# Kernel tuning notes

Hardware: AMD Instinct MI355X
Metric: run time of the kernel (lower is better)

The kernel has to match this reference:

```python
import jax, jax.numpy as jnp
import numpy as np

N, E = 50000, 800000
IN_DIM, HIDDEN, HEADS, EDGE_DIM, OUT_DIM = 128, 64, 4, 16, 1
NEG_SLOPE = 0.2


def gat_conv(x, src, dst, edge_attr, W, We, att_src, att_dst, att_edge, bias, heads, out_ch, concat):
    n = x.shape[0]
    h = (x @ W).reshape(n, heads, out_ch)                     # [N,H,C]
    a_src = jnp.einsum('nhc,hc->nh', h, att_src)              # [N,H]
    a_dst = jnp.einsum('nhc,hc->nh', h, att_dst)
    e = (edge_attr @ We).reshape(-1, heads, out_ch)           # [E,H,C]
    a_e = jnp.einsum('ehc,hc->eh', e, att_edge)               # [E,H]
    alpha = jax.nn.leaky_relu(a_src[src] + a_dst[dst] + a_e, NEG_SLOPE)  # [E,H]
    # per-destination-node softmax
    amax = jax.ops.segment_max(alpha, dst, num_segments=n)
    ex = jnp.exp(alpha - amax[dst])
    denom = jax.ops.segment_sum(ex, dst, num_segments=n)
    alpha = ex / (denom[dst] + 1e-16)
    msg = h[src] * alpha[..., None]                           # [E,H,C]
    out = jax.ops.segment_sum(msg, dst, num_segments=n)       # [N,H,C]
    out = out.reshape(n, heads * out_ch) if concat else out.mean(axis=1)
    return out + bias


def setup_inputs() -> dict:
    key = jax.random.key(0)
    ks = jax.random.split(key, 16)
    s = 0.1
    inp = {
        'x': jax.random.normal(ks[0], (N, IN_DIM), jnp.float32),
        'edge_index': jax.random.randint(ks[1], (2, E), 0, N, jnp.int32),
        'edge_attr': jax.random.normal(ks[2], (E, EDGE_DIM), jnp.float32),
        # layer 1: heads=4, concat=True
        'W1': jax.random.normal(ks[3], (IN_DIM, HEADS * HIDDEN), jnp.float32) * s,
        'We1': jax.random.normal(ks[4], (EDGE_DIM, HEADS * HIDDEN), jnp.float32) * s,
        'as1': jax.random.normal(ks[5], (HEADS, HIDDEN), jnp.float32) * s,
        'ad1': jax.random.normal(ks[6], (HEADS, HIDDEN), jnp.float32) * s,
        'ae1': jax.random.normal(ks[7], (HEADS, HIDDEN), jnp.float32) * s,
        'b1': jnp.zeros((HEADS * HIDDEN,), jnp.float32),
        # layer 2: heads=1, concat=False
        'W2': jax.random.normal(ks[8], (HEADS * HIDDEN, HIDDEN), jnp.float32) * s,
        'We2': jax.random.normal(ks[9], (EDGE_DIM, HIDDEN), jnp.float32) * s,
        'as2': jax.random.normal(ks[10], (1, HIDDEN), jnp.float32) * s,
        'ad2': jax.random.normal(ks[11], (1, HIDDEN), jnp.float32) * s,
        'ae2': jax.random.normal(ks[12], (1, HIDDEN), jnp.float32) * s,
        'b2': jnp.zeros((HIDDEN,), jnp.float32),
        'Wlin': jax.random.normal(ks[13], (HIDDEN, OUT_DIM), jnp.float32) * s,
        'blin': jnp.zeros((OUT_DIM,), jnp.float32),
    }
    return inp


def reference(x, edge_index, edge_attr, W1, We1, as1, ad1, ae1, b1, W2, We2, as2, ad2, ae2, b2, Wlin, blin):
    src, dst = edge_index[0], edge_index[1]
    h = jax.nn.relu(gat_conv(x, src, dst, edge_attr, W1, We1, as1, ad1, ae1, b1, HEADS, HIDDEN, True))
    h = jax.nn.relu(gat_conv(h, src, dst, edge_attr, W2, We2, as2, ad2, ae2, b2, 1, HIDDEN, False))
    return h @ Wlin + blin
```

## Files before the change

kernel.cpp:

```cpp
#include <hip/hip_runtime.h>
#include <math.h>

#define IN_DIM 128
#define HID 64
#define HEADS 4
#define EDGE_DIM 16
#define L1_OUT 256
#define NEG_SLOPE 0.2f
#define PAD 64

typedef __attribute__((ext_vector_type(8))) _Float16 half8_t;
typedef __attribute__((ext_vector_type(4))) _Float16 half4_t;
typedef __attribute__((ext_vector_type(4))) float floatx4;

struct __align__(16) Rec16 {
    int src;
    float aeq2;
    _Float16 e1[4];
};

__global__ __launch_bounds__(256) void prep_kernel(
    const float* __restrict__ W1, const float* __restrict__ as1, const float* __restrict__ ad1,
    const float* __restrict__ W2, const float* __restrict__ as2, const float* __restrict__ ad2,
    const float* __restrict__ We1, const float* __restrict__ ae1,
    const float* __restrict__ We2, const float* __restrict__ ae2,
    _Float16* __restrict__ W1t, _Float16* __restrict__ W2t,
    float* __restrict__ q1, float* __restrict__ q2,
    int* __restrict__ deg, int Nn) {
    int id = blockIdx.x * 256 + threadIdx.x;
    if (id < Nn) deg[id] = 0;
    if (id < 272 * 128) {
        int n = id >> 7, k = id & 127;
        float v = 0.f;
        if (n < 256) v = W1[k * 256 + n];
        else if (n < 260) { int h = n - 256; float s = 0.f;
            for (int c = 0; c < 64; ++c) s += W1[k * 256 + h * 64 + c] * as1[h * 64 + c]; v = s; }
        else if (n < 264) { int h = n - 260; float s = 0.f;
            for (int c = 0; c < 64; ++c) s += W1[k * 256 + h * 64 + c] * ad1[h * 64 + c]; v = s; }
        W1t[id] = (_Float16)v;
        return;
    }
    id -= 272 * 128;
    if (id < 80 * 256) {
        int n = id >> 8, k = id & 255;
        float v = 0.f;
        if (n < 64) v = W2[k * 64 + n];
        else if (n == 64) { float s = 0.f; for (int c = 0; c < 64; ++c) s += W2[k * 64 + c] * as2[c]; v = s; }
        else if (n == 65) { float s = 0.f; for (int c = 0; c < 64; ++c) s += W2[k * 64 + c] * ad2[c]; v = s; }
        W2t[id] = (_Float16)v;
        return;
    }
    id -= 80 * 256;
    if (id < 64) {
        int k = id >> 2, h = id & 3;
        float s = 0.f;
        for (int c = 0; c < 64; ++c) s += We1[k * 256 + h * 64 + c] * ae1[h * 64 + c];
        q1[id] = s;
        return;
    }
    id -= 64;
    if (id < 16) {
        float s = 0.f;
        for (int c = 0; c < 64; ++c) s += We2[id * 64 + c] * ae2[c];
        q2[id] = s;
    }
}

__global__ __launch_bounds__(256) void scatter_edge_kernel(
    const int* __restrict__ src, const int* __restrict__ dst,
    const float* __restrict__ ea, const float* __restrict__ q1,
    const float* __restrict__ q2, const float* __restrict__ asrc1,
    const float* __restrict__ adst1, int* __restrict__ deg,
    floatx4* __restrict__ rec, int E) {
    __shared__ float q[80];
    if (threadIdx.x < 64) q[threadIdx.x] = q1[threadIdx.x];
    else if (threadIdx.x < 80) q[threadIdx.x] = q2[threadIdx.x - 64];
    __syncthreads();
    int e = blockIdx.x * 256 + threadIdx.x;
    if (e >= E) return;
    const floatx4* p = (const floatx4*)(ea + (size_t)e * EDGE_DIM);
    floatx4 v0 = __builtin_nontemporal_load(p);
    floatx4 v1 = __builtin_nontemporal_load(p + 1);
    floatx4 v2 = __builtin_nontemporal_load(p + 2);
    floatx4 v3 = __builtin_nontemporal_load(p + 3);
    int sn = src[e];
    int d = dst[e];
    float4 as4 = *(const float4*)(asrc1 + (size_t)sn * 4);
    float4 ad4 = *(const float4*)(adst1 + (size_t)d * 4);
    float a[16] = {v0.x, v0.y, v0.z, v0.w, v1.x, v1.y, v1.z, v1.w,
                   v2.x, v2.y, v2.z, v2.w, v3.x, v3.y, v3.z, v3.w};
    Rec16 rc;
    rc.src = sn;
    float r2s = 0.f;
#pragma unroll
    for (int k = 0; k < 16; ++k) r2s += a[k] * q[64 + k];
    rc.aeq2 = r2s;
    const float* asp = (const float*)&as4;
    const float* adp = (const float*)&ad4;
#pragma unroll
    for (int h = 0; h < 4; ++h) {
        float s = 0.f;
#pragma unroll
        for (int k = 0; k < 16; ++k) s += a[k] * q[k * 4 + h];
        float tv = s + asp[h] + adp[h];
        rc.e1[h] = (_Float16)__expf(tv > 0.f ? tv : NEG_SLOPE * tv);
    }
    int rank = atomicAdd(&deg[d], 1);
    if (rank >= PAD) return;
    __builtin_nontemporal_store(*(const floatx4*)&rc, rec + (size_t)d * PAD + rank);
}

template <int NTOT, int NFEAT, int HATT, bool A32>
__global__ __launch_bounds__(256) void gemm_att_kernel(
    const void* __restrict__ Av, const _Float16* __restrict__ Bt,
    _Float16* __restrict__ C, float* __restrict__ asrc, float* __restrict__ adst,
    int M, int K) {
    __shared__ _Float16 As[64][72];
    __shared__ _Float16 Bts[NTOT * 16][72];
    const int tid = threadIdx.x;
    const int lane = tid & 63;
    const int w = tid >> 6;
    const int row0 = blockIdx.x * 64;
    const int m = lane & 15;
    const int quad = lane >> 4;

    floatx4 acc[NTOT];
#pragma unroll
    for (int t = 0; t < NTOT; ++t) acc[t] = (floatx4){0.f, 0.f, 0.f, 0.f};

    const int ar = tid >> 2;
    const int ac = (tid & 3) * 16;

    for (int k0 = 0; k0 < K; k0 += 64) {
        half8_t a0 = {}, a1 = {};
        if (row0 + ar < M) {
            if constexpr (A32) {
                const float* A = (const float*)Av + (size_t)(row0 + ar) * K + k0 + ac;
                const float4* f = (const float4*)A;
                float4 f0 = f[0], f1 = f[1], f2 = f[2], f3 = f[3];
                a0 = (half8_t){(_Float16)f0.x, (_Float16)f0.y, (_Float16)f0.z, (_Float16)f0.w,
                               (_Float16)f1.x, (_Float16)f1.y, (_Float16)f1.z, (_Float16)f1.w};
                a1 = (half8_t){(_Float16)f2.x, (_Float16)f2.y, (_Float16)f2.z, (_Float16)f2.w,
                               (_Float16)f3.x, (_Float16)f3.y, (_Float16)f3.z, (_Float16)f3.w};
            } else {
                const half8_t* g = (const half8_t*)((const _Float16*)Av + (size_t)(row0 + ar) * K + k0 + ac);
                a0 = g[0]; a1 = g[1];
            }
        }
        *(half8_t*)&As[ar][ac] = a0;
        *(half8_t*)&As[ar][ac + 8] = a1;
        for (int idx = tid; idx < NTOT * 128; idx += 256) {
            int n = idx >> 3, j = (idx & 7) * 8;
            *(half8_t*)&Bts[n][j] = *(const half8_t*)(Bt + (size_t)n * K + k0 + j);
        }
        __syncthreads();
#pragma unroll
        for (int kc = 0; kc < 2; ++kc) {
            half8_t af = *(const half8_t*)&As[w * 16 + m][kc * 32 + quad * 8];
#pragma unroll
            for (int t = 0; t < NTOT; ++t) {
                half8_t bf = *(const half8_t*)&Bts[t * 16 + m][kc * 32 + quad * 8];
                acc[t] = __builtin_amdgcn_mfma_f32_16x16x32_f16(af, bf, acc[t], 0, 0, 0);
            }
        }
        __syncthreads();
    }
    const int TE = NFEAT / 16;
#pragma unroll
    for (int r = 0; r < 4; ++r) {
        int row = row0 + w * 16 + quad * 4 + r;
        if (row >= M) continue;
#pragma unroll
        for (int t = 0; t < TE; ++t)
            C[(size_t)row * NFEAT + t * 16 + m] = (_Float16)acc[t][r];
        float v = acc[TE][r];
        if (m < HATT) asrc[row * HATT + m] = v;
        else if (m < 2 * HATT) adst[row * HATT + (m - HATT)] = v;
    }
}

__global__ __launch_bounds__(256) void node1_kernel(
    const int* __restrict__ deg, const floatx4* __restrict__ rec,
    const _Float16* __restrict__ h1, const float* __restrict__ b1,
    _Float16* __restrict__ hr1, int Nn) {
    int lane = threadIdx.x & 63, wv = threadIdx.x >> 6;
    int n = blockIdx.x * 4 + wv;
    if (n >= Nn) return;
    int dg = __builtin_amdgcn_readfirstlane(deg[n]);
    if (dg > PAD) dg = PAD;
    size_t s0 = (size_t)n * PAD, s1 = s0 + dg;
    const int hh = lane >> 4;
    const int* reci = (const int*)rec;
    const _Float16* rech = (const _Float16*)rec;

    float ax = 0.f, ay = 0.f, az = 0.f, aw = 0.f, l = 0.f;
    size_t s = s0;
    for (; s + 7 < s1; s += 8) {
        int idx[8];
        float ew[8];
        half4_t v[8];
#pragma unroll
        for (int j = 0; j < 8; ++j) idx[j] = reci[(s + j) * 4];
#pragma unroll
        for (int j = 0; j < 8; ++j) ew[j] = (float)rech[(s + j) * 8 + 4 + hh];
#pragma unroll
        for (int j = 0; j < 8; ++j)
            v[j] = *(const half4_t*)(h1 + (size_t)idx[j] * L1_OUT + lane * 4);
#pragma unroll
        for (int j = 0; j < 8; ++j) {
            l += ew[j];
            ax += ew[j] * (float)v[j].x;
            ay += ew[j] * (float)v[j].y;
            az += ew[j] * (float)v[j].z;
            aw += ew[j] * (float)v[j].w;
        }
    }
    for (; s < s1; ++s) {
        int i0 = reci[s * 4];
        float e0 = (float)rech[s * 8 + 4 + hh];
        half4_t v0 = *(const half4_t*)(h1 + (size_t)i0 * L1_OUT + lane * 4);
        l += e0;
        ax += e0 * (float)v0.x; ay += e0 * (float)v0.y;
        az += e0 * (float)v0.z; aw += e0 * (float)v0.w;
    }
    float inv = 1.f / (l + 1e-16f);
    float4 bb = *(const float4*)(b1 + lane * 4);
    half4_t out;
    out.x = (_Float16)fmaxf(ax * inv + bb.x, 0.f);
    out.y = (_Float16)fmaxf(ay * inv + bb.y, 0.f);
    out.z = (_Float16)fmaxf(az * inv + bb.z, 0.f);
    out.w = (_Float16)fmaxf(aw * inv + bb.w, 0.f);
    *(half4_t*)(hr1 + (size_t)n * L1_OUT + lane * 4) = out;
}

__global__ __launch_bounds__(256) void node2_kernel(
    const int* __restrict__ deg, const floatx4* __restrict__ rec,
    const float* __restrict__ asrc2, const float* __restrict__ adst2,
    const _Float16* __restrict__ h2, const float* __restrict__ b2,
    const float* __restrict__ Wlin, const float* __restrict__ blin,
    float* __restrict__ out, int Nn) {
    int lane = threadIdx.x & 63, wv = threadIdx.x >> 6;
    int n = blockIdx.x * 4 + wv;
    if (n >= Nn) return;
    int dg = __builtin_amdgcn_readfirstlane(deg[n]);
    if (dg > PAD) dg = PAD;
    size_t s0 = (size_t)n * PAD, s1 = s0 + dg;
    float adn = adst2[n];
    const int* reci = (const int*)rec;
    const float* recf = (const float*)rec;

    float l = 0.f, acc = 0.f;
    size_t s = s0;
    for (; s + 7 < s1; s += 8) {
        int idx[8];
        float aq[8], asv[8], v[8];
#pragma unroll
        for (int j = 0; j < 8; ++j) idx[j] = reci[(s + j) * 4];
#pragma unroll
        for (int j = 0; j < 8; ++j) aq[j] = recf[(s + j) * 4 + 1];
#pragma unroll
        for (int j = 0; j < 8; ++j) asv[j] = asrc2[idx[j]];
#pragma unroll
        for (int j = 0; j < 8; ++j) v[j] = (float)h2[(size_t)idx[j] * HID + lane];
#pragma unroll
        for (int j = 0; j < 8; ++j) {
            float t = aq[j] + asv[j] + adn;
            float e = __expf(t > 0.f ? t : NEG_SLOPE * t);
            l += e;
            acc += e * v[j];
        }
    }
    for (; s < s1; ++s) {
        int n0 = reci[s * 4];
        float t0 = recf[s * 4 + 1] + asrc2[n0] + adn;
        float e0 = __expf(t0 > 0.f ? t0 : NEG_SLOPE * t0);
        float v0 = (float)h2[(size_t)n0 * HID + lane];
        l += e0;
        acc += e0 * v0;
    }
    float res = fmaxf(acc / (l + 1e-16f) + b2[lane], 0.f);
    float t = res * Wlin[lane];
    for (int o = 32; o > 0; o >>= 1) t += __shfl_down(t, o);
    if (lane == 0) out[n] = t + blin[0];
}

extern "C" void kernel_launch(void* const* d_in, const int* in_sizes, int n_in,
                              void* d_out, int out_size, void* d_ws, size_t ws_size,
                              hipStream_t stream) {
    const float* x    = (const float*)d_in[0];
    const int*   ei   = (const int*)d_in[1];
    const float* ea   = (const float*)d_in[2];
    const float* W1   = (const float*)d_in[3];
    const float* We1  = (const float*)d_in[4];
    const float* as1  = (const float*)d_in[5];
    const float* ad1  = (const float*)d_in[6];
    const float* ae1  = (const float*)d_in[7];
    const float* b1   = (const float*)d_in[8];
    const float* W2   = (const float*)d_in[9];
    const float* We2  = (const float*)d_in[10];
    const float* as2  = (const float*)d_in[11];
    const float* ad2  = (const float*)d_in[12];
    const float* ae2  = (const float*)d_in[13];
    const float* b2   = (const float*)d_in[14];
    const float* Wlin = (const float*)d_in[15];
    const float* blin = (const float*)d_in[16];

    const int N = in_sizes[0] / IN_DIM;
    const int E = in_sizes[1] / 2;
    const int* src = ei;
    const int* dst = ei + E;

    char* base = (char*)d_ws;
    size_t off = 0;
    auto alloc = [&](size_t bytes) -> char* {
        char* p = base + off;
        off = (off + bytes + 255) & ~(size_t)255;
        return p;
    };
    int*      deg     = (int*)alloc((size_t)N * 4);
    float*    q1      = (float*)alloc(64 * 4);
    float*    q2      = (float*)alloc(16 * 4);
    _Float16* W1t     = (_Float16*)alloc((size_t)272 * 128 * 2);
    _Float16* W2t     = (_Float16*)alloc((size_t)80 * 256 * 2);
    floatx4*  rec     = (floatx4*)alloc((size_t)N * PAD * 16);
    float*    asrc1   = (float*)alloc((size_t)N * 4 * 4);
    float*    adst1   = (float*)alloc((size_t)N * 4 * 4);
    _Float16* h1      = (_Float16*)alloc((size_t)N * L1_OUT * 2);
    _Float16* hr1     = (_Float16*)alloc((size_t)N * L1_OUT * 2);
    _Float16* h2      = (_Float16*)alloc((size_t)N * HID * 2);
    float*    asrc2   = (float*)alloc((size_t)N * 4);
    float*    adst2   = (float*)alloc((size_t)N * 4);
    (void)ws_size; (void)n_in; (void)out_size;

    prep_kernel<<<218, 256, 0, stream>>>(W1, as1, ad1, W2, as2, ad2,
                                         We1, ae1, We2, ae2, W1t, W2t, q1, q2, deg, N);

    int mbl = (N + 63) / 64;
    gemm_att_kernel<17, 256, 4, true><<<mbl, 256, 0, stream>>>(x, W1t, h1, asrc1, adst1,
                                                               N, IN_DIM);
    scatter_edge_kernel<<<(E + 255) / 256, 256, 0, stream>>>(src, dst, ea, q1, q2,
                                                             asrc1, adst1, deg, rec, E);
    node1_kernel<<<(N + 3) / 4, 256, 0, stream>>>(deg, rec, h1, b1, hr1, N);
    gemm_att_kernel<5, 64, 1, false><<<mbl, 256, 0, stream>>>(hr1, W2t, h2, asrc2, adst2,
                                                              N, L1_OUT);
    node2_kernel<<<(N + 3) / 4, 256, 0, stream>>>(deg, rec, asrc2, adst2, h2, b2,
                                                  Wlin, blin, (float*)d_out, N);
}
```

Measured before the change: 335.4 us.

## Move edge-attribute projection into prep kernel ahead of layer-1 GEMM

The per-edge projections of edge_attr onto the attention vectors are now computed in the prep kernel, launched over all edges, and written to new per-edge buffers. Every prep block also recomputes the small q vectors into shared memory. The scatter kernel then reads 20 bytes per edge instead of the 64-byte edge_attr row. This takes the edge_attr read out of the scatter kernel, but it adds an extra write and read of the intermediate buffers, redundant q computation in each block, and prep now has to finish before the GEMM starts.

```diff
diff --git a/kernel.cpp b/kernel.cpp
--- a/kernel.cpp
+++ b/kernel.cpp
@@ -24,11 +24,28 @@
     const float* __restrict__ W2, const float* __restrict__ as2, const float* __restrict__ ad2,
     const float* __restrict__ We1, const float* __restrict__ ae1,
     const float* __restrict__ We2, const float* __restrict__ ae2,
+    const float* __restrict__ ea,
     _Float16* __restrict__ W1t, _Float16* __restrict__ W2t,
-    float* __restrict__ q1, float* __restrict__ q2,
-    int* __restrict__ deg, int Nn) {
-    int id = blockIdx.x * 256 + threadIdx.x;
+    float* __restrict__ aeqA, float* __restrict__ aeqB,
+    int* __restrict__ deg, int Nn, int E) {
+    __shared__ float q[80];
+    int tid = threadIdx.x;
+    if (tid < 64) {
+        int k = tid >> 2, h = tid & 3;
+        float s = 0.f;
+        for (int c = 0; c < 64; ++c) s += We1[k * 256 + h * 64 + c] * ae1[h * 64 + c];
+        q[tid] = s;
+    } else if (tid < 80) {
+        int k = tid - 64;
+        float s = 0.f;
+        for (int c = 0; c < 64; ++c) s += We2[k * 64 + c] * ae2[c];
+        q[tid] = s;
+    }
+    __syncthreads();
+
+    int id = blockIdx.x * 256 + tid;
     if (id < Nn) deg[id] = 0;
+
     if (id < 272 * 128) {
         int n = id >> 7, k = id & 127;
         float v = 0.f;
@@ -38,71 +55,64 @@
         else if (n < 264) { int h = n - 260; float s = 0.f;
             for (int c = 0; c < 64; ++c) s += W1[k * 256 + h * 64 + c] * ad1[h * 64 + c]; v = s; }
         W1t[id] = (_Float16)v;
-        return;
-    }
-    id -= 272 * 128;
-    if (id < 80 * 256) {
-        int n = id >> 8, k = id & 255;
+    } else if (id < 272 * 128 + 80 * 256) {
+        int id2 = id - 272 * 128;
+        int n = id2 >> 8, k = id2 & 255;
         float v = 0.f;
         if (n < 64) v = W2[k * 64 + n];
         else if (n == 64) { float s = 0.f; for (int c = 0; c < 64; ++c) s += W2[k * 64 + c] * as2[c]; v = s; }
         else if (n == 65) { float s = 0.f; for (int c = 0; c < 64; ++c) s += W2[k * 64 + c] * ad2[c]; v = s; }
-        W2t[id] = (_Float16)v;
-        return;
-    }
-    id -= 80 * 256;
-    if (id < 64) {
-        int k = id >> 2, h = id & 3;
-        float s = 0.f;
-        for (int c = 0; c < 64; ++c) s += We1[k * 256 + h * 64 + c] * ae1[h * 64 + c];
-        q1[id] = s;
-        return;
-    }
-    id -= 64;
-    if (id < 16) {
-        float s = 0.f;
-        for (int c = 0; c < 64; ++c) s += We2[id * 64 + c] * ae2[c];
-        q2[id] = s;
+        W2t[id2] = (_Float16)v;
+    }
+
+    if (id < E) {
+        const floatx4* p = (const floatx4*)(ea + (size_t)id * EDGE_DIM);
+        floatx4 v0 = __builtin_nontemporal_load(p);
+        floatx4 v1 = __builtin_nontemporal_load(p + 1);
+        floatx4 v2 = __builtin_nontemporal_load(p + 2);
+        floatx4 v3 = __builtin_nontemporal_load(p + 3);
+        float a[16] = {v0.x, v0.y, v0.z, v0.w, v1.x, v1.y, v1.z, v1.w,
+                       v2.x, v2.y, v2.z, v2.w, v3.x, v3.y, v3.z, v3.w};
+        floatx4 r1;
+        float rp[4];
+#pragma unroll
+        for (int h = 0; h < 4; ++h) {
+            float s = 0.f;
+#pragma unroll
+            for (int k = 0; k < 16; ++k) s += a[k] * q[k * 4 + h];
+            rp[h] = s;
+        }
+        r1.x = rp[0]; r1.y = rp[1]; r1.z = rp[2]; r1.w = rp[3];
+        float r2 = 0.f;
+#pragma unroll
+        for (int k = 0; k < 16; ++k) r2 += a[k] * q[64 + k];
+        __builtin_nontemporal_store(r1, (floatx4*)aeqA + id);
+        __builtin_nontemporal_store(r2, aeqB + id);
     }
 }
 
 __global__ __launch_bounds__(256) void scatter_edge_kernel(
     const int* __restrict__ src, const int* __restrict__ dst,
-    const float* __restrict__ ea, const float* __restrict__ q1,
-    const float* __restrict__ q2, const float* __restrict__ asrc1,
-    const float* __restrict__ adst1, int* __restrict__ deg,
-    floatx4* __restrict__ rec, int E) {
-    __shared__ float q[80];
-    if (threadIdx.x < 64) q[threadIdx.x] = q1[threadIdx.x];
-    else if (threadIdx.x < 80) q[threadIdx.x] = q2[threadIdx.x - 64];
-    __syncthreads();
+    const float* __restrict__ aeqA, const float* __restrict__ aeqB,
+    const float* __restrict__ asrc1, const float* __restrict__ adst1,
+    int* __restrict__ deg, floatx4* __restrict__ rec, int E) {
     int e = blockIdx.x * 256 + threadIdx.x;
     if (e >= E) return;
-    const floatx4* p = (const floatx4*)(ea + (size_t)e * EDGE_DIM);
-    floatx4 v0 = __builtin_nontemporal_load(p);
-    floatx4 v1 = __builtin_nontemporal_load(p + 1);
-    floatx4 v2 = __builtin_nontemporal_load(p + 2);
-    floatx4 v3 = __builtin_nontemporal_load(p + 3);
+    floatx4 aq = __builtin_nontemporal_load((const floatx4*)aeqA + e);
+    float ab = __builtin_nontemporal_load(aeqB + e);
     int sn = src[e];
     int d = dst[e];
     float4 as4 = *(const float4*)(asrc1 + (size_t)sn * 4);
     float4 ad4 = *(const float4*)(adst1 + (size_t)d * 4);
-    float a[16] = {v0.x, v0.y, v0.z, v0.w, v1.x, v1.y, v1.z, v1.w,
-                   v2.x, v2.y, v2.z, v2.w, v3.x, v3.y, v3.z, v3.w};
+    float aqv[4] = {aq.x, aq.y, aq.z, aq.w};
+    const float* asp = (const float*)&as4;
+    const float* adp = (const float*)&ad4;
     Rec16 rc;
     rc.src = sn;
-    float r2s = 0.f;
-#pragma unroll
-    for (int k = 0; k < 16; ++k) r2s += a[k] * q[64 + k];
-    rc.aeq2 = r2s;
-    const float* asp = (const float*)&as4;
-    const float* adp = (const float*)&ad4;
+    rc.aeq2 = ab;
 #pragma unroll
     for (int h = 0; h < 4; ++h) {
-        float s = 0.f;
-#pragma unroll
-        for (int k = 0; k < 16; ++k) s += a[k] * q[k * 4 + h];
-        float tv = s + asp[h] + adp[h];
+        float tv = aqv[h] + asp[h] + adp[h];
         rc.e1[h] = (_Float16)__expf(tv > 0.f ? tv : NEG_SLOPE * tv);
     }
     int rank = atomicAdd(&deg[d], 1);
@@ -318,11 +328,11 @@
         return p;
     };
     int*      deg     = (int*)alloc((size_t)N * 4);
-    float*    q1      = (float*)alloc(64 * 4);
-    float*    q2      = (float*)alloc(16 * 4);
     _Float16* W1t     = (_Float16*)alloc((size_t)272 * 128 * 2);
     _Float16* W2t     = (_Float16*)alloc((size_t)80 * 256 * 2);
     floatx4*  rec     = (floatx4*)alloc((size_t)N * PAD * 16);
+    float*    aeqA    = (float*)alloc((size_t)E * 16);
+    float*    aeqB    = (float*)alloc((size_t)E * 4);
     float*    asrc1   = (float*)alloc((size_t)N * 4 * 4);
     float*    adst1   = (float*)alloc((size_t)N * 4 * 4);
     _Float16* h1      = (_Float16*)alloc((size_t)N * L1_OUT * 2);
@@ -332,14 +342,16 @@
     float*    adst2   = (float*)alloc((size_t)N * 4);
     (void)ws_size; (void)n_in; (void)out_size;
 
-    prep_kernel<<<218, 256, 0, stream>>>(W1, as1, ad1, W2, as2, ad2,
-                                         We1, ae1, We2, ae2, W1t, W2t, q1, q2, deg, N);
+    int ebl = (E + 255) / 256;
+    prep_kernel<<<ebl, 256, 0, stream>>>(W1, as1, ad1, W2, as2, ad2,
+                                         We1, ae1, We2, ae2, ea,
+                                         W1t, W2t, aeqA, aeqB, deg, N, E);
 
     int mbl = (N + 63) / 64;
     gemm_att_kernel<17, 256, 4, true><<<mbl, 256, 0, stream>>>(x, W1t, h1, asrc1, adst1,
                                                                N, IN_DIM);
-    scatter_edge_kernel<<<(E + 255) / 256, 256, 0, stream>>>(src, dst, ea, q1, q2,
-                                                             asrc1, adst1, deg, rec, E);
+    scatter_edge_kernel<<<ebl, 256, 0, stream>>>(src, dst, aeqA, aeqB,
+                                                 asrc1, adst1, deg, rec, E);
     node1_kernel<<<(N + 3) / 4, 256, 0, stream>>>(deg, rec, h1, b1, hr1, N);
     gemm_att_kernel<5, 64, 1, false><<<mbl, 256, 0, stream>>>(hr1, W2t, h2, asrc2, adst2,
                                                               N, L1_OUT);
```

After: 357.3 us. 6.5% more time.
